# Kernel optimization log

Hardware: AMD Instinct MI355X
Metric: run time of the kernel (lower is better)

The kernel has to match this reference:

```python
import math
import jax, jax.numpy as jnp
import numpy as np

T = 4096
D_MODEL = 1024
NUM_HEADS = 16
HEAD_DIM = D_MODEL // NUM_HEADS


def setup_inputs() -> dict:
    key = jax.random.key(0)
    k_x, k_wqkv, k_wproj = jax.random.split(key, 3)
    # match eqx.nn.Linear init scale: U(-1/sqrt(in), 1/sqrt(in)); randn*small works too,
    # but keep magnitudes reasonable so softmax isn't saturated.
    s_in = 1.0 / math.sqrt(D_MODEL)
    x = jax.random.normal(k_x, (T, D_MODEL), dtype=jnp.float32)
    W_qkv = jax.random.normal(k_wqkv, (3 * D_MODEL, D_MODEL), dtype=jnp.float32) * s_in
    b_qkv = jnp.zeros((3 * D_MODEL,), dtype=jnp.float32)
    W_proj = jax.random.normal(k_wproj, (D_MODEL, D_MODEL), dtype=jnp.float32) * s_in
    b_proj = jnp.zeros((D_MODEL,), dtype=jnp.float32)
    return {"x": x, "W_qkv": W_qkv, "b_qkv": b_qkv, "W_proj": W_proj, "b_proj": b_proj}


def reference(x, W_qkv, b_qkv, W_proj, b_proj):
    T_, C = x.shape  # (seq, d_model)
    H, hd = NUM_HEADS, HEAD_DIM
    # c_attn: eqx Linear computes W @ x + b per token -> x @ W.T + b
    qkv = x @ W_qkv.T + b_qkv  # (T, 3C)
    q, k, v = jnp.split(qkv, 3, axis=1)
    # (T, C) -> (H, T, hd)
    q = q.reshape(T_, H, hd).swapaxes(0, 1)
    k = k.reshape(T_, H, hd).swapaxes(0, 1)
    v = v.reshape(T_, H, hd).swapaxes(0, 1)
    scores = jnp.einsum("htd,hsd->hts", q, k) / math.sqrt(hd)  # (H, T, T)
    causal = jnp.tril(jnp.ones((T_, T_), dtype=bool))
    scores = jnp.where(causal, scores, -jnp.inf)
    attn = jax.nn.softmax(scores, axis=-1)
    y = jnp.einsum("hts,hsd->htd", attn, v)  # (H, T, hd)
    y = y.swapaxes(0, 1).reshape(T_, C)
    y = y @ W_proj.T + b_proj
    return y
```

## Files before the change

### kernel.cpp

```cpp
#include <hip/hip_runtime.h>
#include <math.h>
#include <string.h>

#define T_SEQ 4096
#define DM 1024
#define NH 16
#define HD 64

typedef short s8v __attribute__((ext_vector_type(8)));
typedef float f4v __attribute__((ext_vector_type(4)));

__device__ inline unsigned short f2bf(float f) {
    unsigned u; memcpy(&u, &f, 4);
    u = u + 0x7fffu + ((u >> 16) & 1u);
    return (unsigned short)(u >> 16);
}

__device__ inline float bf2f(unsigned short s) {
    unsigned u = (unsigned)s << 16;
    float f; memcpy(&f, &u, 4);
    return f;
}

__device__ inline float exp2fn(float x) {
#if __has_builtin(__builtin_amdgcn_exp2f)
    return __builtin_amdgcn_exp2f(x);
#else
    return exp2f(x);
#endif
}

__device__ inline void gld_lds16(const void* g, void* l) {
    __builtin_amdgcn_global_load_lds(
        (const __attribute__((address_space(1))) void*)g,
        (__attribute__((address_space(3))) void*)l, 16, 0, 0);
}

__global__ __launch_bounds__(256)
void cvt3(const float* __restrict__ i0, unsigned short* __restrict__ o0, int n0,
          const float* __restrict__ i1, unsigned short* __restrict__ o1, int n1,
          const float* __restrict__ i2, unsigned short* __restrict__ o2, int n2) {
    int i = blockIdx.x * 256 + threadIdx.x;
    const float* in; unsigned short* out; int j;
    if (i < n0)           { in = i0; out = o0; j = i; }
    else if (i < n0 + n1) { in = i1; out = o1; j = i - n0; }
    else if (i < n0 + n1 + n2) { in = i2; out = o2; j = i - n0 - n1; }
    else return;
    const float4* p = (const float4*)(in + (size_t)j * 8);
    float4 a = p[0], b = p[1];
    unsigned short o[8] = {f2bf(a.x), f2bf(a.y), f2bf(a.z), f2bf(a.w),
                           f2bf(b.x), f2bf(b.y), f2bf(b.z), f2bf(b.w)};
    uint4 pk; memcpy(&pk, o, 16);
    *(uint4*)(out + (size_t)j * 8) = pk;
}

template<int MODE, int TN>
__global__ __launch_bounds__(256)
void gemm_bt_mfma(const unsigned short* __restrict__ A, const unsigned short* __restrict__ B,
                  const float* __restrict__ bias, void* __restrict__ Cout,
                  unsigned short* __restrict__ qbuf, unsigned short* __restrict__ kbuf2,
                  unsigned short* __restrict__ vT,
                  int M, int N, int K, int nbx, int patchw, int patchh) {
    constexpr int NF = TN / 32;
    __shared__ __align__(16) short As[2][4096];
    __shared__ __align__(16) short Bs[2][TN * 32];
    const int tid = threadIdx.x;
    const int w = tid >> 6, lane = tid & 63;
    const int wr = w >> 1, wc = w & 1;

    const int bl = blockIdx.x;
    const int xcd = bl & 7, ii = bl >> 3;
    const int pxn = nbx / patchw;
    const int bx = (xcd % pxn) * patchw + ii % patchw;
    const int by = (xcd / pxn) * patchh + ii / patchw;
    const int m0 = by * 128, n0 = bx * TN;

    const bool doA = (w < 2);
    const bool doStage = doA || ((w & 1) * 64 < TN);
    const unsigned short* src = doA ? A : B;
    const int rbase = (doA ? m0 : n0) + (w & 1) * 64;
    const unsigned short* gsrc = src + (size_t)(rbase + (lane & 15)) * K + ((lane >> 4) * 8);
    const int ldoff = ((w & 1) * 4) * 512;

    f4v acc[4][NF];
    #pragma unroll
    for (int i = 0; i < 4; ++i)
        #pragma unroll
        for (int j = 0; j < NF; ++j) acc[i][j] = (f4v){0.f, 0.f, 0.f, 0.f};

    auto stage = [&](short* base, int k0) {
        short* ldst = base + ldoff;
        #pragma unroll
        for (int i = 0; i < 4; ++i)
            gld_lds16(gsrc + (size_t)(i * 16) * K + k0, ldst + i * 512);
    };
    auto compute = [&](const short* Ab, const short* Bb) {
        s8v af[4], bfr[NF];
        #pragma unroll
        for (int i = 0; i < 4; ++i) af[i] = *(const s8v*)&Ab[((wr * 4 + i) * 64 + lane) * 8];
        #pragma unroll
        for (int j = 0; j < NF; ++j) bfr[j] = *(const s8v*)&Bb[((wc * NF + j) * 64 + lane) * 8];
        #pragma unroll
        for (int i = 0; i < 4; ++i)
            #pragma unroll
            for (int j = 0; j < NF; ++j)
                acc[i][j] = __builtin_amdgcn_mfma_f32_16x16x32_bf16(af[i], bfr[j], acc[i][j], 0, 0, 0);
    };

    if (doStage) stage(doA ? As[0] : Bs[0], 0);
    __syncthreads();
    for (int k0 = 0; k0 < K; k0 += 64) {
        if (doStage) stage(doA ? As[1] : Bs[1], k0 + 32);
        compute(As[0], Bs[0]);
        __syncthreads();
        if (doStage && (k0 + 64 < K)) stage(doA ? As[0] : Bs[0], k0 + 64);
        compute(As[1], Bs[1]);
        __syncthreads();
    }

    const int l15 = lane & 15, quad = lane >> 4;
    float bj[NF];
    #pragma unroll
    for (int j = 0; j < NF; ++j) bj[j] = bias[n0 + wc * (TN / 2) + j * 16 + l15];

    if (MODE == 2 && n0 >= 2 * DM) {
        const int tile = (m0 + wr * 64) >> 6;
        const int hh = ((n0 - 2 * DM) >> 6) + wc;
        #pragma unroll
        for (int i = 0; i < 4; ++i) {
            #pragma unroll
            for (int j = 0; j < NF; ++j) {
                unsigned short o[4];
                #pragma unroll
                for (int rg = 0; rg < 4; ++rg) o[rg] = f2bf(acc[i][j][rg] + bj[j]);
                unsigned long long pk; memcpy(&pk, o, 8);
                size_t off = (size_t)hh * 262144 + (size_t)tile * 4096
                           + (size_t)((j * 2 + (i >> 1)) * 64 + lane) * 8 + (i & 1) * 4;
                *(unsigned long long*)&vT[off] = pk;
            }
        }
    } else if (MODE == 2) {
        unsigned short* dst = (n0 < DM) ? qbuf : kbuf2;
        const int nb = (n0 < DM) ? n0 : n0 - DM;
        #pragma unroll
        for (int i = 0; i < 4; ++i) {
            #pragma unroll
            for (int rg = 0; rg < 4; ++rg) {
                int row = m0 + wr * 64 + i * 16 + quad * 4 + rg;
                #pragma unroll
                for (int j = 0; j < NF; ++j) {
                    int col = nb + wc * (TN / 2) + j * 16 + l15;
                    dst[(size_t)row * DM + col] = f2bf(acc[i][j][rg] + bj[j]);
                }
            }
        }
    } else {
        #pragma unroll
        for (int i = 0; i < 4; ++i) {
            #pragma unroll
            for (int rg = 0; rg < 4; ++rg) {
                int row = m0 + wr * 64 + i * 16 + quad * 4 + rg;
                #pragma unroll
                for (int j = 0; j < NF; ++j) {
                    int col = n0 + wc * (TN / 2) + j * 16 + l15;
                    ((float*)Cout)[(size_t)row * N + col] = acc[i][j][rg] + bj[j];
                }
            }
        }
    }
}

__device__ __forceinline__ void soft_step(f4v* st, bool diag, int qloc, int quad,
                                          float& lr, s8v& pf0, s8v& pf1) {
    const float C2  = 0.1803368851f;
    const float MC2 = 12.0f * 0.1803368851f;
    float sv[4][4];
    #pragma unroll
    for (int kb = 0; kb < 4; ++kb)
        #pragma unroll
        for (int rg = 0; rg < 4; ++rg) {
            float s = st[kb][rg];
            if (diag && (kb * 16 + quad * 4 + rg > qloc)) s = -3.0e38f;
            float t = exp2fn(fmaf(s, C2, -MC2));
            sv[kb][rg] = t;
            lr += t;
        }
    int pk[4][2];
    #pragma unroll
    for (int kb = 0; kb < 4; ++kb) {
        unsigned u0 = __float_as_uint(sv[kb][0]) + 0x8000u;
        unsigned u1 = __float_as_uint(sv[kb][1]) + 0x8000u;
        unsigned u2 = __float_as_uint(sv[kb][2]) + 0x8000u;
        unsigned u3 = __float_as_uint(sv[kb][3]) + 0x8000u;
        pk[kb][0] = (int)__builtin_amdgcn_perm(u1, u0, 0x07060302);
        pk[kb][1] = (int)__builtin_amdgcn_perm(u3, u2, 0x07060302);
    }
    int4 a = {pk[0][0], pk[0][1], pk[1][0], pk[1][1]};
    int4 b = {pk[2][0], pk[2][1], pk[3][0], pk[3][1]};
    memcpy(&pf0, &a, 16);
    memcpy(&pf1, &b, 16);
}

__global__ __launch_bounds__(256, 3)
void attn_mfma7(const unsigned short* __restrict__ qb,
                const unsigned short* __restrict__ kbf,
                const unsigned short* __restrict__ vT,
                unsigned short* __restrict__ y0,
                unsigned short* __restrict__ y1,
                unsigned short* __restrict__ y2,
                float* __restrict__ lsum) {
    const int b = blockIdx.x;
    const int par = b % 3;
    const int idx = b / 3;
    const int h = idx & 15, a = idx >> 4;
    const int tid = threadIdx.x;
    const int w = tid >> 6, lane = tid & 63;
    const int quad = lane >> 4, l15 = lane & 15;
    const int cq = h * HD;
    unsigned short* ypar = (par == 0) ? y0 : (par == 1) ? y1 : y2;
    float* lpar = lsum + ((size_t)par * NH + h) * T_SEQ;
    const unsigned short* vbase = vT + (size_t)h * 262144;

    __shared__ short KB[2][4096];
    __shared__ short VTs[2][4096];
    __shared__ short QB[8192];

    for (int ph = 0; ph < 2; ++ph) {
        const int qt = ph ? (31 - a) : a;
        const int q0 = qt * 128;
        const int kmax = 2 * qt + 1;
        const int nk = (kmax >= par) ? (kmax - par) / 3 + 1 : 0;
        const int kt0 = par * 64;

        __syncthreads();
        #pragma unroll
        for (int rr = 0; rr < 4; ++rr) {
            int ch = rr * 256 + tid;
            int qg = ch >> 7, hf = (ch >> 6) & 1, ln = ch & 63;
            gld_lds16(qb + (size_t)(q0 + qg * 16 + (ln & 15)) * DM + cq + hf * 32 + ((ln >> 4) << 3),
                      &QB[(ch & ~63) * 8]);
        }
        if (nk > 0) {
            #pragma unroll
            for (int rr = 0; rr < 2; ++rr) {
                int ch = rr * 256 + tid;
                int blk = ch >> 7, hf = (ch >> 6) & 1, ln = ch & 63;
                gld_lds16(kbf + (size_t)(kt0 + blk * 16 + (ln & 15)) * DM + cq + hf * 32 + ((ln >> 4) << 3),
                          &KB[0][(ch & ~63) * 8]);
                gld_lds16(vbase + (size_t)(kt0 >> 6) * 4096 + (size_t)ch * 8,
                          &VTs[0][(ch & ~63) * 8]);
            }
        }
        __syncthreads();

        s8v qf[2][2];
        #pragma unroll
        for (int g = 0; g < 2; ++g)
            #pragma unroll
            for (int hf = 0; hf < 2; ++hf)
                qf[g][hf] = *(const s8v*)&QB[((((g * 4 + w) * 2 + hf) * 64) + lane) * 8];

        f4v O0[4], O1[4];
        #pragma unroll
        for (int ob = 0; ob < 4; ++ob) {
            O0[ob] = (f4v){0.f, 0.f, 0.f, 0.f};
            O1[ob] = (f4v){0.f, 0.f, 0.f, 0.f};
        }
        float lr0 = 0.f, lr1 = 0.f;

        for (int i = 0; i < nk; ++i) {
            const int kt = par + 3 * i;
            const int p = i & 1;
            const bool g0a = (kt <= 2 * qt);
            const bool m0 = (kt == 2 * qt);
            const bool m1 = (kt == 2 * qt + 1);
            if (i < nk - 1) {
                const int k1 = kt0 + (i + 1) * 192;
                #pragma unroll
                for (int rr = 0; rr < 2; ++rr) {
                    int ch = rr * 256 + tid;
                    int blk = ch >> 7, hf = (ch >> 6) & 1, ln = ch & 63;
                    gld_lds16(kbf + (size_t)(k1 + blk * 16 + (ln & 15)) * DM + cq
                                  + hf * 32 + ((ln >> 4) << 3),
                              &KB[p ^ 1][(ch & ~63) * 8]);
                    gld_lds16(vbase + (size_t)(k1 >> 6) * 4096 + (size_t)ch * 8,
                              &VTs[p ^ 1][(ch & ~63) * 8]);
                }
            }

            f4v st0[4], st1[4];
            #pragma unroll
            for (int kb = 0; kb < 4; ++kb) {
                s8v k0f = *(const s8v*)&KB[p][((kb * 2 + 0) * 64 + lane) * 8];
                s8v k1f = *(const s8v*)&KB[p][((kb * 2 + 1) * 64 + lane) * 8];
                f4v c1 = (f4v){0.f, 0.f, 0.f, 0.f};
                c1 = __builtin_amdgcn_mfma_f32_16x16x32_bf16(k0f, qf[1][0], c1, 0, 0, 0);
                c1 = __builtin_amdgcn_mfma_f32_16x16x32_bf16(k1f, qf[1][1], c1, 0, 0, 0);
                st1[kb] = c1;
                if (g0a) {
                    f4v c0 = (f4v){0.f, 0.f, 0.f, 0.f};
                    c0 = __builtin_amdgcn_mfma_f32_16x16x32_bf16(k0f, qf[0][0], c0, 0, 0, 0);
                    c0 = __builtin_amdgcn_mfma_f32_16x16x32_bf16(k1f, qf[0][1], c0, 0, 0, 0);
                    st0[kb] = c0;
                }
            }

            s8v pf10, pf11, pf00, pf01;
            soft_step(st1, m1, w * 16 + l15, quad, lr1, pf10, pf11);
            if (g0a) soft_step(st0, m0, w * 16 + l15, quad, lr0, pf00, pf01);

            #pragma unroll
            for (int ob = 0; ob < 4; ++ob) {
                s8v v0f = *(const s8v*)&VTs[p][((ob * 2 + 0) * 64 + lane) * 8];
                s8v v1f = *(const s8v*)&VTs[p][((ob * 2 + 1) * 64 + lane) * 8];
                O1[ob] = __builtin_amdgcn_mfma_f32_16x16x32_bf16(v0f, pf10, O1[ob], 0, 0, 0);
                O1[ob] = __builtin_amdgcn_mfma_f32_16x16x32_bf16(v1f, pf11, O1[ob], 0, 0, 0);
                if (g0a) {
                    O0[ob] = __builtin_amdgcn_mfma_f32_16x16x32_bf16(v0f, pf00, O0[ob], 0, 0, 0);
                    O0[ob] = __builtin_amdgcn_mfma_f32_16x16x32_bf16(v1f, pf01, O0[ob], 0, 0, 0);
                }
            }
            __syncthreads();
        }

        lr0 += __shfl_xor(lr0, 16); lr0 += __shfl_xor(lr0, 32);
        lr1 += __shfl_xor(lr1, 16); lr1 += __shfl_xor(lr1, 32);
        #pragma unroll
        for (int g = 0; g < 2; ++g) {
            const f4v* O = g ? O1 : O0;
            int qrow = q0 + g * 64 + w * 16 + l15;
            size_t ybase = (size_t)qrow * DM + cq;
            #pragma unroll
            for (int ob = 0; ob < 4; ++ob) {
                unsigned short o[4];
                #pragma unroll
                for (int rg = 0; rg < 4; ++rg) o[rg] = f2bf(O[ob][rg]);
                unsigned long long pk; memcpy(&pk, o, 8);
                *(unsigned long long*)&ypar[ybase + ob * 16 + quad * 4] = pk;
            }
            if (quad == 0) lpar[qrow] = g ? lr1 : lr0;
        }
    }
}

__global__ __launch_bounds__(256)
void attn_combine3(const unsigned short* __restrict__ y0,
                   const unsigned short* __restrict__ y1,
                   const unsigned short* __restrict__ y2,
                   const float* __restrict__ lsum,
                   unsigned short* __restrict__ yout) {
    int i = blockIdx.x * 256 + threadIdx.x;
    int t = i >> 7, d8 = i & 127;
    int h = d8 >> 3;
    float l = lsum[(size_t)h * T_SEQ + t]
            + lsum[((size_t)NH + h) * T_SEQ + t]
            + lsum[((size_t)2 * NH + h) * T_SEQ + t];
    float inv = 1.f / l;
    size_t off = (size_t)t * DM + d8 * 8;
    uint4 ua = *(const uint4*)(y0 + off);
    uint4 ub = *(const uint4*)(y1 + off);
    uint4 uc = *(const uint4*)(y2 + off);
    const unsigned short* pa = (const unsigned short*)&ua;
    const unsigned short* pb = (const unsigned short*)&ub;
    const unsigned short* pc = (const unsigned short*)&uc;
    unsigned short o[8];
    #pragma unroll
    for (int k = 0; k < 8; ++k)
        o[k] = f2bf((bf2f(pa[k]) + bf2f(pb[k]) + bf2f(pc[k])) * inv);
    uint4 pk; memcpy(&pk, o, 16);
    *(uint4*)(yout + off) = pk;
}

extern "C" void kernel_launch(void* const* d_in, const int* in_sizes, int n_in,
                              void* d_out, int out_size, void* d_ws, size_t ws_size,
                              hipStream_t stream) {
    const float* x     = (const float*)d_in[0];
    const float* Wqkv  = (const float*)d_in[1];
    const float* bqkv  = (const float*)d_in[2];
    const float* Wproj = (const float*)d_in[3];
    const float* bproj = (const float*)d_in[4];
    float* out = (float*)d_out;

    char* ws = (char*)d_ws;
    unsigned short* qbuf  = (unsigned short*)(ws);
    unsigned short* kbuf  = (unsigned short*)(ws + ( 8u << 20));
    unsigned short* vTb   = (unsigned short*)(ws + (16u << 20));
    unsigned short* yattb = (unsigned short*)(ws + (24u << 20));
    unsigned short* wprjb = (unsigned short*)(ws + (32u << 20));
    float*          lsum  = (float*)         (ws + (34u << 20));
    unsigned short* xb    = (unsigned short*)(ws + (35u << 20));
    unsigned short* wqkvb = (unsigned short*)(ws + (43u << 20));
    unsigned short* y0p   = (unsigned short*)(ws + (35u << 20));
    unsigned short* y1p   = (unsigned short*)(ws + (43u << 20));
    unsigned short* y2p   = (unsigned short*)(ws + (51u << 20));

    dim3 blk(256);
    {
        int n0 = T_SEQ * DM / 8, n1 = 3 * DM * DM / 8, n2 = DM * DM / 8;
        cvt3<<<dim3((n0 + n1 + n2 + 255) / 256), blk, 0, stream>>>(
            x, xb, n0, Wqkv, wqkvb, n1, Wproj, wprjb, n2);
    }
    gemm_bt_mfma<2, 128><<<dim3(768), blk, 0, stream>>>(
        xb, wqkvb, bqkv, nullptr, qbuf, kbuf, vTb, T_SEQ, 3 * DM, DM, 24, 6, 16);
    attn_mfma7<<<dim3(768), blk, 0, stream>>>(qbuf, kbuf, vTb, y0p, y1p, y2p, lsum);
    attn_combine3<<<dim3(T_SEQ * DM / 8 / 256), blk, 0, stream>>>(y0p, y1p, y2p, lsum, yattb);
    gemm_bt_mfma<0, 64><<<dim3(512), blk, 0, stream>>>(
        yattb, wprjb, bproj, out, nullptr, nullptr, nullptr, T_SEQ, DM, DM, 16, 8, 8);
}
```

Before: 215.7 us.

## Split-K output projection with atomics and narrower QKV GEMM tiles

Output projection now uses split-K by 2 with atomic float adds into an output pre-filled with bias by a new init kernel, doubling the block count. The QKV GEMM switches to 64-wide N tiles with 1536 blocks and an occupancy hint of 6, and the V-transpose store indexing is adapted for the narrower tile. This aims to raise parallelism and occupancy on the GEMMs at the cost of atomic traffic, an extra launch, and a stray dummy LDS read in compute.

```diff
diff --git a/kernel.cpp b/kernel.cpp
--- a/kernel.cpp
+++ b/kernel.cpp
@@ -54,13 +54,21 @@
     *(uint4*)(out + (size_t)j * 8) = pk;
 }
 
-template<int MODE, int TN>
 __global__ __launch_bounds__(256)
+void binit(const float* __restrict__ bias, float* __restrict__ out) {
+    int i = blockIdx.x * 256 + threadIdx.x;
+    int col4 = (i & (DM / 4 - 1)) * 4;
+    float4 b = *(const float4*)&bias[col4];
+    *(float4*)&out[(size_t)i * 4] = b;
+}
+
+template<int MODE, int TN, int OCC>
+__global__ __launch_bounds__(256, OCC)
 void gemm_bt_mfma(const unsigned short* __restrict__ A, const unsigned short* __restrict__ B,
                   const float* __restrict__ bias, void* __restrict__ Cout,
                   unsigned short* __restrict__ qbuf, unsigned short* __restrict__ kbuf2,
                   unsigned short* __restrict__ vT,
-                  int M, int N, int K, int nbx, int patchw, int patchh) {
+                  int M, int N, int K, int nbx, int patchw, int patchh, int kspl) {
     constexpr int NF = TN / 32;
     __shared__ __align__(16) short As[2][4096];
     __shared__ __align__(16) short Bs[2][TN * 32];
@@ -68,7 +76,10 @@
     const int w = tid >> 6, lane = tid & 63;
     const int wr = w >> 1, wc = w & 1;
 
-    const int bl = blockIdx.x;
+    const int bpk = 8 * patchw * patchh;
+    const int s = blockIdx.x / bpk;
+    const int bl = blockIdx.x % bpk;
+    const int ks = s * (K / kspl), ke = ks + K / kspl;
     const int xcd = bl & 7, ii = bl >> 3;
     const int pxn = nbx / patchw;
     const int bx = (xcd % pxn) * patchw + ii % patchw;
@@ -99,6 +110,8 @@
         #pragma unroll
         for (int i = 0; i < 4; ++i) af[i] = *(const s8v*)&Ab[((wr * 4 + i) * 64 + lane) * 8];
         #pragma unroll
+        for (int j = 0; j < NF; ++j) bfr[j] = *(const s8v*)&Bs[0][0];
+        #pragma unroll
         for (int j = 0; j < NF; ++j) bfr[j] = *(const s8v*)&Bb[((wc * NF + j) * 64 + lane) * 8];
         #pragma unroll
         for (int i = 0; i < 4; ++i)
@@ -107,39 +120,43 @@
                 acc[i][j] = __builtin_amdgcn_mfma_f32_16x16x32_bf16(af[i], bfr[j], acc[i][j], 0, 0, 0);
     };
 
-    if (doStage) stage(doA ? As[0] : Bs[0], 0);
+    if (doStage) stage(doA ? As[0] : Bs[0], ks);
     __syncthreads();
-    for (int k0 = 0; k0 < K; k0 += 64) {
+    for (int k0 = ks; k0 < ke; k0 += 64) {
         if (doStage) stage(doA ? As[1] : Bs[1], k0 + 32);
         compute(As[0], Bs[0]);
         __syncthreads();
-        if (doStage && (k0 + 64 < K)) stage(doA ? As[0] : Bs[0], k0 + 64);
+        if (doStage && (k0 + 64 < ke)) stage(doA ? As[0] : Bs[0], k0 + 64);
         compute(As[1], Bs[1]);
         __syncthreads();
     }
 
     const int l15 = lane & 15, quad = lane >> 4;
-    float bj[NF];
-    #pragma unroll
-    for (int j = 0; j < NF; ++j) bj[j] = bias[n0 + wc * (TN / 2) + j * 16 + l15];
 
     if (MODE == 2 && n0 >= 2 * DM) {
+        float bj[NF];
+        #pragma unroll
+        for (int j = 0; j < NF; ++j) bj[j] = bias[n0 + wc * (TN / 2) + j * 16 + l15];
         const int tile = (m0 + wr * 64) >> 6;
-        const int hh = ((n0 - 2 * DM) >> 6) + wc;
+        const int hh = ((n0 - 2 * DM) >> 6) + (TN == 128 ? wc : 0);
         #pragma unroll
         for (int i = 0; i < 4; ++i) {
             #pragma unroll
             for (int j = 0; j < NF; ++j) {
+                const int ob = (TN == 128) ? j : (wc * 2 + j);
                 unsigned short o[4];
                 #pragma unroll
                 for (int rg = 0; rg < 4; ++rg) o[rg] = f2bf(acc[i][j][rg] + bj[j]);
                 unsigned long long pk; memcpy(&pk, o, 8);
                 size_t off = (size_t)hh * 262144 + (size_t)tile * 4096
-                           + (size_t)((j * 2 + (i >> 1)) * 64 + lane) * 8 + (i & 1) * 4;
+                           + (size_t)((ob * 2 + (i >> 1)) * 64 + lane) * 8 + (i & 1) * 4;
                 *(unsigned long long*)&vT[off] = pk;
             }
         }
     } else if (MODE == 2) {
+        float bj[NF];
+        #pragma unroll
+        for (int j = 0; j < NF; ++j) bj[j] = bias[n0 + wc * (TN / 2) + j * 16 + l15];
         unsigned short* dst = (n0 < DM) ? qbuf : kbuf2;
         const int nb = (n0 < DM) ? n0 : n0 - DM;
         #pragma unroll
@@ -154,7 +171,24 @@
                 }
             }
         }
+    } else if (MODE == 3) {
+        float* outp = (float*)Cout;
+        #pragma unroll
+        for (int i = 0; i < 4; ++i) {
+            #pragma unroll
+            for (int rg = 0; rg < 4; ++rg) {
+                int row = m0 + wr * 64 + i * 16 + quad * 4 + rg;
+                #pragma unroll
+                for (int j = 0; j < NF; ++j) {
+                    int col = n0 + wc * (TN / 2) + j * 16 + l15;
+                    unsafeAtomicAdd(&outp[(size_t)row * N + col], acc[i][j][rg]);
+                }
+            }
+        }
     } else {
+        float bj[NF];
+        #pragma unroll
+        for (int j = 0; j < NF; ++j) bj[j] = bias[n0 + wc * (TN / 2) + j * 16 + l15];
         #pragma unroll
         for (int i = 0; i < 4; ++i) {
             #pragma unroll
@@ -386,10 +420,10 @@
     unsigned short* kbuf  = (unsigned short*)(ws + ( 8u << 20));
     unsigned short* vTb   = (unsigned short*)(ws + (16u << 20));
     unsigned short* yattb = (unsigned short*)(ws + (24u << 20));
-    unsigned short* wprjb = (unsigned short*)(ws + (32u << 20));
     float*          lsum  = (float*)         (ws + (34u << 20));
     unsigned short* xb    = (unsigned short*)(ws + (35u << 20));
     unsigned short* wqkvb = (unsigned short*)(ws + (43u << 20));
+    unsigned short* wprjb = (unsigned short*)(ws + (32u << 20));
     unsigned short* y0p   = (unsigned short*)(ws + (35u << 20));
     unsigned short* y1p   = (unsigned short*)(ws + (43u << 20));
     unsigned short* y2p   = (unsigned short*)(ws + (51u << 20));
@@ -400,10 +434,11 @@
         cvt3<<<dim3((n0 + n1 + n2 + 255) / 256), blk, 0, stream>>>(
             x, xb, n0, Wqkv, wqkvb, n1, Wproj, wprjb, n2);
     }
-    gemm_bt_mfma<2, 128><<<dim3(768), blk, 0, stream>>>(
-        xb, wqkvb, bqkv, nullptr, qbuf, kbuf, vTb, T_SEQ, 3 * DM, DM, 24, 6, 16);
+    binit<<<dim3(T_SEQ * DM / 4 / 256), blk, 0, stream>>>(bproj, out);
+    gemm_bt_mfma<2, 64, 6><<<dim3(1536), blk, 0, stream>>>(
+        xb, wqkvb, bqkv, nullptr, qbuf, kbuf, vTb, T_SEQ, 3 * DM, DM, 48, 24, 8, 1);
     attn_mfma7<<<dim3(768), blk, 0, stream>>>(qbuf, kbuf, vTb, y0p, y1p, y2p, lsum);
     attn_combine3<<<dim3(T_SEQ * DM / 8 / 256), blk, 0, stream>>>(y0p, y1p, y2p, lsum, yattb);
-    gemm_bt_mfma<0, 64><<<dim3(512), blk, 0, stream>>>(
-        yattb, wprjb, bproj, out, nullptr, nullptr, nullptr, T_SEQ, DM, DM, 16, 8, 8);
-}
+    gemm_bt_mfma<3, 64, 4><<<dim3(1024), blk, 0, stream>>>(
+        yattb, wprjb, bproj, out, nullptr, nullptr, nullptr, T_SEQ, DM, DM, 16, 8, 8, 2);
+}
```

Result: slower. 260.8 us (+20.9%).

## Replace double-buffered GEMM staging with single-buffer K=64 stages and occupancy hints

Applied to the files above, without the earlier changes.

The GEMM kernel drops its two-stage ping-pong LDS buffering and instead loads a full 64-wide K slab into a single buffer per iteration, with a sync before and after staging. It adds a min-blocks-per-CU launch bound (3 for the QKV GEMM, 2 for the projection), and for TN=64 it spreads B staging across both B waves by K half. The aim is to rely on higher occupancy rather than intra-block double buffering to hide load latency, with fewer syncs per K step. The cost is that loads no longer overlap compute within a block, and the launch bounds may limit registers.

```diff
diff --git a/kernel.cpp b/kernel.cpp
--- a/kernel.cpp
+++ b/kernel.cpp
@@ -54,16 +54,16 @@
     *(uint4*)(out + (size_t)j * 8) = pk;
 }
 
-template<int MODE, int TN>
-__global__ __launch_bounds__(256)
+template<int MODE, int TN, int OCC>
+__global__ __launch_bounds__(256, OCC)
 void gemm_bt_mfma(const unsigned short* __restrict__ A, const unsigned short* __restrict__ B,
                   const float* __restrict__ bias, void* __restrict__ Cout,
                   unsigned short* __restrict__ qbuf, unsigned short* __restrict__ kbuf2,
                   unsigned short* __restrict__ vT,
                   int M, int N, int K, int nbx, int patchw, int patchh) {
     constexpr int NF = TN / 32;
-    __shared__ __align__(16) short As[2][4096];
-    __shared__ __align__(16) short Bs[2][TN * 32];
+    __shared__ __align__(16) short As[8192];
+    __shared__ __align__(16) short Bs[TN * 64];
     const int tid = threadIdx.x;
     const int w = tid >> 6, lane = tid & 63;
     const int wr = w >> 1, wc = w & 1;
@@ -75,12 +75,10 @@
     const int by = (xcd / pxn) * patchh + ii / patchw;
     const int m0 = by * 128, n0 = bx * TN;
 
-    const bool doA = (w < 2);
-    const bool doStage = doA || ((w & 1) * 64 < TN);
-    const unsigned short* src = doA ? A : B;
-    const int rbase = (doA ? m0 : n0) + (w & 1) * 64;
-    const unsigned short* gsrc = src + (size_t)(rbase + (lane & 15)) * K + ((lane >> 4) * 8);
-    const int ldoff = ((w & 1) * 4) * 512;
+    const unsigned short* gA = A + (size_t)(m0 + (w & 1) * 64 + (lane & 15)) * K + ((lane >> 4) * 8);
+    const unsigned short* gB =
+        (TN == 128) ? B + (size_t)(n0 + (w & 1) * 64 + (lane & 15)) * K + ((lane >> 4) * 8)
+                    : B + (size_t)(n0 + (lane & 15)) * K + ((lane >> 4) * 8);
 
     f4v acc[4][NF];
     #pragma unroll
@@ -88,58 +86,82 @@
         #pragma unroll
         for (int j = 0; j < NF; ++j) acc[i][j] = (f4v){0.f, 0.f, 0.f, 0.f};
 
-    auto stage = [&](short* base, int k0) {
-        short* ldst = base + ldoff;
-        #pragma unroll
-        for (int i = 0; i < 4; ++i)
-            gld_lds16(gsrc + (size_t)(i * 16) * K + k0, ldst + i * 512);
+    auto stage = [&](int k0) {
+        if (w < 2) {
+            #pragma unroll
+            for (int kh = 0; kh < 2; ++kh)
+                #pragma unroll
+                for (int i = 0; i < 4; ++i)
+                    gld_lds16(gA + (size_t)(i * 16) * K + k0 + kh * 32,
+                              &As[kh * 4096 + ((w & 1) * 4 + i) * 512]);
+        } else if constexpr (TN == 128) {
+            #pragma unroll
+            for (int kh = 0; kh < 2; ++kh)
+                #pragma unroll
+                for (int i = 0; i < 4; ++i)
+                    gld_lds16(gB + (size_t)(i * 16) * K + k0 + kh * 32,
+                              &Bs[kh * 4096 + ((w & 1) * 4 + i) * 512]);
+        } else {
+            const int kh = w & 1;
+            #pragma unroll
+            for (int i = 0; i < 4; ++i)
+                gld_lds16(gB + (size_t)(i * 16) * K + k0 + kh * 32,
+                          &Bs[kh * 2048 + i * 512]);
+        }
     };
-    auto compute = [&](const short* Ab, const short* Bb) {
-        s8v af[4], bfr[NF];
-        #pragma unroll
-        for (int i = 0; i < 4; ++i) af[i] = *(const s8v*)&Ab[((wr * 4 + i) * 64 + lane) * 8];
-        #pragma unroll
-        for (int j = 0; j < NF; ++j) bfr[j] = *(const s8v*)&Bb[((wc * NF + j) * 64 + lane) * 8];
-        #pragma unroll
-        for (int i = 0; i < 4; ++i)
+    auto compute = [&]() {
+        s8v af[2][4], bfr[2][NF];
+        #pragma unroll
+        for (int kh = 0; kh < 2; ++kh) {
+            #pragma unroll
+            for (int i = 0; i < 4; ++i)
+                af[kh][i] = *(const s8v*)&As[kh * 4096 + ((wr * 4 + i) * 64 + lane) * 8];
             #pragma unroll
             for (int j = 0; j < NF; ++j)
-                acc[i][j] = __builtin_amdgcn_mfma_f32_16x16x32_bf16(af[i], bfr[j], acc[i][j], 0, 0, 0);
+                bfr[kh][j] = *(const s8v*)&Bs[kh * TN * 32 + ((wc * NF + j) * 64 + lane) * 8];
+        }
+        #pragma unroll
+        for (int kh = 0; kh < 2; ++kh)
+            #pragma unroll
+            for (int i = 0; i < 4; ++i)
+                #pragma unroll
+                for (int j = 0; j < NF; ++j)
+                    acc[i][j] = __builtin_amdgcn_mfma_f32_16x16x32_bf16(af[kh][i], bfr[kh][j], acc[i][j], 0, 0, 0);
     };
 
-    if (doStage) stage(doA ? As[0] : Bs[0], 0);
-    __syncthreads();
     for (int k0 = 0; k0 < K; k0 += 64) {
-        if (doStage) stage(doA ? As[1] : Bs[1], k0 + 32);
-        compute(As[0], Bs[0]);
         __syncthreads();
-        if (doStage && (k0 + 64 < K)) stage(doA ? As[0] : Bs[0], k0 + 64);
-        compute(As[1], Bs[1]);
+        stage(k0);
         __syncthreads();
+        compute();
     }
 
     const int l15 = lane & 15, quad = lane >> 4;
-    float bj[NF];
-    #pragma unroll
-    for (int j = 0; j < NF; ++j) bj[j] = bias[n0 + wc * (TN / 2) + j * 16 + l15];
 
     if (MODE == 2 && n0 >= 2 * DM) {
+        float bj[NF];
+        #pragma unroll
+        for (int j = 0; j < NF; ++j) bj[j] = bias[n0 + wc * (TN / 2) + j * 16 + l15];
         const int tile = (m0 + wr * 64) >> 6;
-        const int hh = ((n0 - 2 * DM) >> 6) + wc;
+        const int hh = ((n0 - 2 * DM) >> 6) + (TN == 128 ? wc : 0);
         #pragma unroll
         for (int i = 0; i < 4; ++i) {
             #pragma unroll
             for (int j = 0; j < NF; ++j) {
+                const int ob = (TN == 128) ? j : (wc * 2 + j);
                 unsigned short o[4];
                 #pragma unroll
                 for (int rg = 0; rg < 4; ++rg) o[rg] = f2bf(acc[i][j][rg] + bj[j]);
                 unsigned long long pk; memcpy(&pk, o, 8);
                 size_t off = (size_t)hh * 262144 + (size_t)tile * 4096
-                           + (size_t)((j * 2 + (i >> 1)) * 64 + lane) * 8 + (i & 1) * 4;
+                           + (size_t)((ob * 2 + (i >> 1)) * 64 + lane) * 8 + (i & 1) * 4;
                 *(unsigned long long*)&vT[off] = pk;
             }
         }
     } else if (MODE == 2) {
+        float bj[NF];
+        #pragma unroll
+        for (int j = 0; j < NF; ++j) bj[j] = bias[n0 + wc * (TN / 2) + j * 16 + l15];
         unsigned short* dst = (n0 < DM) ? qbuf : kbuf2;
         const int nb = (n0 < DM) ? n0 : n0 - DM;
         #pragma unroll
@@ -155,6 +177,9 @@
             }
         }
     } else {
+        float bj[NF];
+        #pragma unroll
+        for (int j = 0; j < NF; ++j) bj[j] = bias[n0 + wc * (TN / 2) + j * 16 + l15];
         #pragma unroll
         for (int i = 0; i < 4; ++i) {
             #pragma unroll
@@ -400,10 +425,10 @@
         cvt3<<<dim3((n0 + n1 + n2 + 255) / 256), blk, 0, stream>>>(
             x, xb, n0, Wqkv, wqkvb, n1, Wproj, wprjb, n2);
     }
-    gemm_bt_mfma<2, 128><<<dim3(768), blk, 0, stream>>>(
+    gemm_bt_mfma<2, 128, 3><<<dim3(768), blk, 0, stream>>>(
         xb, wqkvb, bqkv, nullptr, qbuf, kbuf, vTb, T_SEQ, 3 * DM, DM, 24, 6, 16);
     attn_mfma7<<<dim3(768), blk, 0, stream>>>(qbuf, kbuf, vTb, y0p, y1p, y2p, lsum);
     attn_combine3<<<dim3(T_SEQ * DM / 8 / 256), blk, 0, stream>>>(y0p, y1p, y2p, lsum, yattb);
-    gemm_bt_mfma<0, 64><<<dim3(512), blk, 0, stream>>>(
+    gemm_bt_mfma<0, 64, 2><<<dim3(512), blk, 0, stream>>>(
         yattb, wprjb, bproj, out, nullptr, nullptr, nullptr, T_SEQ, DM, DM, 16, 8, 8);
 }
```

Result: slower. 221.1 us (+2.5%).

## Replace LDS-staged GEMM with direct global-to-register fragment loads

Applied to the files above, without the earlier changes.

The two projection GEMMs no longer stage A/B tiles through shared memory with barriers. Each wave now loads its MFMA fragments straight from global memory into registers, double-buffered in registers, and launch bounds carry an occupancy hint. This removes the LDS traffic and __syncthreads overhead, at the cost of redundant global/L2 reads, since tiles are no longer shared across waves, and higher register pressure. The V-transpose epilogue is generalised for TN=64.

```diff
diff --git a/kernel.cpp b/kernel.cpp
--- a/kernel.cpp
+++ b/kernel.cpp
@@ -54,19 +54,18 @@
     *(uint4*)(out + (size_t)j * 8) = pk;
 }
 
-template<int MODE, int TN>
-__global__ __launch_bounds__(256)
-void gemm_bt_mfma(const unsigned short* __restrict__ A, const unsigned short* __restrict__ B,
-                  const float* __restrict__ bias, void* __restrict__ Cout,
-                  unsigned short* __restrict__ qbuf, unsigned short* __restrict__ kbuf2,
-                  unsigned short* __restrict__ vT,
-                  int M, int N, int K, int nbx, int patchw, int patchh) {
+template<int MODE, int TN, int OCC>
+__global__ __launch_bounds__(256, OCC)
+void gemm_bt_reg(const unsigned short* __restrict__ A, const unsigned short* __restrict__ B,
+                 const float* __restrict__ bias, void* __restrict__ Cout,
+                 unsigned short* __restrict__ qbuf, unsigned short* __restrict__ kbuf2,
+                 unsigned short* __restrict__ vT,
+                 int M, int N, int K, int nbx, int patchw, int patchh) {
     constexpr int NF = TN / 32;
-    __shared__ __align__(16) short As[2][4096];
-    __shared__ __align__(16) short Bs[2][TN * 32];
     const int tid = threadIdx.x;
     const int w = tid >> 6, lane = tid & 63;
     const int wr = w >> 1, wc = w & 1;
+    const int l15 = lane & 15, quad = lane >> 4;
 
     const int bl = blockIdx.x;
     const int xcd = bl & 7, ii = bl >> 3;
@@ -75,12 +74,8 @@
     const int by = (xcd / pxn) * patchh + ii / patchw;
     const int m0 = by * 128, n0 = bx * TN;
 
-    const bool doA = (w < 2);
-    const bool doStage = doA || ((w & 1) * 64 < TN);
-    const unsigned short* src = doA ? A : B;
-    const int rbase = (doA ? m0 : n0) + (w & 1) * 64;
-    const unsigned short* gsrc = src + (size_t)(rbase + (lane & 15)) * K + ((lane >> 4) * 8);
-    const int ldoff = ((w & 1) * 4) * 512;
+    const unsigned short* baseA = A + (size_t)(m0 + wr * 64 + l15) * K + quad * 8;
+    const unsigned short* baseB = B + (size_t)(n0 + wc * (TN / 2) + l15) * K + quad * 8;
 
     f4v acc[4][NF];
     #pragma unroll
@@ -88,58 +83,55 @@
         #pragma unroll
         for (int j = 0; j < NF; ++j) acc[i][j] = (f4v){0.f, 0.f, 0.f, 0.f};
 
-    auto stage = [&](short* base, int k0) {
-        short* ldst = base + ldoff;
+    auto ldfrag = [&](s8v* a, s8v* b, int k0) {
         #pragma unroll
         for (int i = 0; i < 4; ++i)
-            gld_lds16(gsrc + (size_t)(i * 16) * K + k0, ldst + i * 512);
+            a[i] = *(const s8v*)(baseA + (size_t)(i * 16) * K + k0);
+        #pragma unroll
+        for (int j = 0; j < NF; ++j)
+            b[j] = *(const s8v*)(baseB + (size_t)(j * 16) * K + k0);
     };
-    auto compute = [&](const short* Ab, const short* Bb) {
-        s8v af[4], bfr[NF];
-        #pragma unroll
-        for (int i = 0; i < 4; ++i) af[i] = *(const s8v*)&Ab[((wr * 4 + i) * 64 + lane) * 8];
-        #pragma unroll
-        for (int j = 0; j < NF; ++j) bfr[j] = *(const s8v*)&Bb[((wc * NF + j) * 64 + lane) * 8];
+    auto mfma16 = [&](const s8v* a, const s8v* b) {
         #pragma unroll
         for (int i = 0; i < 4; ++i)
             #pragma unroll
             for (int j = 0; j < NF; ++j)
-                acc[i][j] = __builtin_amdgcn_mfma_f32_16x16x32_bf16(af[i], bfr[j], acc[i][j], 0, 0, 0);
+                acc[i][j] = __builtin_amdgcn_mfma_f32_16x16x32_bf16(a[i], b[j], acc[i][j], 0, 0, 0);
     };
 
-    if (doStage) stage(doA ? As[0] : Bs[0], 0);
-    __syncthreads();
+    s8v aC[4], bC[NF], aN[4], bN[NF];
+    ldfrag(aC, bC, 0);
     for (int k0 = 0; k0 < K; k0 += 64) {
-        if (doStage) stage(doA ? As[1] : Bs[1], k0 + 32);
-        compute(As[0], Bs[0]);
-        __syncthreads();
-        if (doStage && (k0 + 64 < K)) stage(doA ? As[0] : Bs[0], k0 + 64);
-        compute(As[1], Bs[1]);
-        __syncthreads();
+        ldfrag(aN, bN, k0 + 32);
+        mfma16(aC, bC);
+        if (k0 + 64 < K) ldfrag(aC, bC, k0 + 64);
+        mfma16(aN, bN);
     }
 
-    const int l15 = lane & 15, quad = lane >> 4;
-    float bj[NF];
-    #pragma unroll
-    for (int j = 0; j < NF; ++j) bj[j] = bias[n0 + wc * (TN / 2) + j * 16 + l15];
-
     if (MODE == 2 && n0 >= 2 * DM) {
+        float bj[NF];
+        #pragma unroll
+        for (int j = 0; j < NF; ++j) bj[j] = bias[n0 + wc * (TN / 2) + j * 16 + l15];
         const int tile = (m0 + wr * 64) >> 6;
-        const int hh = ((n0 - 2 * DM) >> 6) + wc;
+        const int hh = ((n0 - 2 * DM) >> 6) + (TN == 128 ? wc : 0);
         #pragma unroll
         for (int i = 0; i < 4; ++i) {
             #pragma unroll
             for (int j = 0; j < NF; ++j) {
+                const int ob = (TN == 128) ? j : (wc * 2 + j);
                 unsigned short o[4];
                 #pragma unroll
                 for (int rg = 0; rg < 4; ++rg) o[rg] = f2bf(acc[i][j][rg] + bj[j]);
                 unsigned long long pk; memcpy(&pk, o, 8);
                 size_t off = (size_t)hh * 262144 + (size_t)tile * 4096
-                           + (size_t)((j * 2 + (i >> 1)) * 64 + lane) * 8 + (i & 1) * 4;
+                           + (size_t)((ob * 2 + (i >> 1)) * 64 + lane) * 8 + (i & 1) * 4;
                 *(unsigned long long*)&vT[off] = pk;
             }
         }
     } else if (MODE == 2) {
+        float bj[NF];
+        #pragma unroll
+        for (int j = 0; j < NF; ++j) bj[j] = bias[n0 + wc * (TN / 2) + j * 16 + l15];
         unsigned short* dst = (n0 < DM) ? qbuf : kbuf2;
         const int nb = (n0 < DM) ? n0 : n0 - DM;
         #pragma unroll
@@ -155,6 +147,9 @@
             }
         }
     } else {
+        float bj[NF];
+        #pragma unroll
+        for (int j = 0; j < NF; ++j) bj[j] = bias[n0 + wc * (TN / 2) + j * 16 + l15];
         #pragma unroll
         for (int i = 0; i < 4; ++i) {
             #pragma unroll
@@ -400,10 +395,10 @@
         cvt3<<<dim3((n0 + n1 + n2 + 255) / 256), blk, 0, stream>>>(
             x, xb, n0, Wqkv, wqkvb, n1, Wproj, wprjb, n2);
     }
-    gemm_bt_mfma<2, 128><<<dim3(768), blk, 0, stream>>>(
+    gemm_bt_reg<2, 128, 3><<<dim3(768), blk, 0, stream>>>(
         xb, wqkvb, bqkv, nullptr, qbuf, kbuf, vTb, T_SEQ, 3 * DM, DM, 24, 6, 16);
     attn_mfma7<<<dim3(768), blk, 0, stream>>>(qbuf, kbuf, vTb, y0p, y1p, y2p, lsum);
     attn_combine3<<<dim3(T_SEQ * DM / 8 / 256), blk, 0, stream>>>(y0p, y1p, y2p, lsum, yattb);
-    gemm_bt_mfma<0, 64><<<dim3(512), blk, 0, stream>>>(
+    gemm_bt_reg<0, 64, 2><<<dim3(512), blk, 0, stream>>>(
         yattb, wprjb, bproj, out, nullptr, nullptr, nullptr, T_SEQ, DM, DM, 16, 8, 8);
 }
```

After: 277.3 us. +28.5%, slower.
